# Kernel tuning notes

Measured on AMD Instinct MI355X. Metric: run time of the kernel, lower is better.

## Reference

```python
import jax, jax.numpy as jnp
import numpy as np

D_MODEL = 1024
K = 256
AMPLITUDE_MAX = 3.0
GATE_BIAS_INIT = 0.65  # alpha-gate bias initialized at logit(0.65)


def setup_inputs() -> dict:
    key = jax.random.key(0)
    k0, k1, k2, k3 = jax.random.split(key, 4)
    B, n = 4, 4096
    x = jax.random.normal(k0, (B, n, D_MODEL), dtype=jnp.float32)
    # OscillatorProjection: Linear(d_model -> 6K), chunks [A, omega, phi, alpha, g, beta]
    W_proj = jax.random.normal(k1, (6 * K, D_MODEL), dtype=jnp.float32) * 0.02
    b_proj = jnp.zeros((6 * K,), dtype=jnp.float32)
    alpha_bias = float(np.log(GATE_BIAS_INIT / (1.0 - GATE_BIAS_INIT)))
    b_proj = b_proj.at[3 * K:4 * K].set(alpha_bias)
    W_res = jax.random.normal(k2, (D_MODEL, 4 * K - 2), dtype=jnp.float32) * 0.002
    W_phase = jax.random.normal(k3, (K, D_MODEL), dtype=jnp.float32) * 0.001
    b_phase = jnp.zeros((K,), dtype=jnp.float32)
    return {
        "x": x, "W_proj": W_proj, "b_proj": b_proj, "W_res": W_res,
        "W_phase": W_phase, "b_phase": b_phase,
        "lambda_pcg": jnp.float32(0.1), "res_scale": jnp.float32(0.05),
    }


def _scan_combine(c1, c2):
    # first-order linear recurrence r_t = a_t * r_{t-1} + b_t (complex, split re/im)
    a1, br1, bi1 = c1
    a2, br2, bi2 = c2
    return (a1 * a2, a2 * br1 + br2, a2 * bi1 + bi2)


def _forward(x, W_proj, b_proj, W_res, W_phase, b_phase, lambda_pcg, res_scale):
    B, n, _ = x.shape
    # OscillatorProjection
    proj = jnp.einsum('bnd,kd->bnk', x, W_proj) + b_proj  # (B, n, 6K)
    a_raw, w_raw, p_raw, al_raw, g_raw, be_raw = jnp.split(proj, 6, axis=-1)
    A = AMPLITUDE_MAX * jax.nn.sigmoid(a_raw)
    omega = jax.nn.softplus(w_raw)
    phi = p_raw
    alpha = jax.nn.sigmoid(al_raw)
    g_out = jax.nn.sigmoid(g_raw)
    beta = jax.nn.sigmoid(be_raw)

    # phase_mode == 'log'
    positions = jnp.log1p(jnp.arange(n, dtype=jnp.float32)).reshape(1, n, 1)
    angle = omega * positions + phi
    cos_a = jnp.cos(angle)
    sin_a = jnp.sin(angle)
    one_m_a = 1.0 - alpha
    drive_r = one_m_a * A * cos_a
    drive_i = one_m_a * A * sin_a

    # parallel associative prefix scan over sequence axis
    _, r_r, r_i = jax.lax.associative_scan(_scan_combine, (alpha, drive_r, drive_i), axis=1)

    # erase (read-and-subtract)
    readout = r_r * cos_a + r_i * sin_a
    r_r = r_r - beta * readout * cos_a
    r_i = r_i - beta * readout * sin_a

    # state norm: r /= max(|r|, 1)
    modulus = jnp.sqrt(r_r * r_r + r_i * r_i + 1e-8)
    scale = jnp.maximum(modulus, 1.0)
    r_r = r_r / scale
    r_i = r_i / scale

    # demodulate: rho = r * exp(-j * angle)
    rho_re = r_r * cos_a + r_i * sin_a
    rho_im = -r_r * sin_a + r_i * cos_a

    # phase-coherence gate
    rho_norm = jnp.sqrt(rho_re * rho_re + rho_im * rho_im + 1e-8)
    phase_query = jnp.einsum('bnd,kd->bnk', x, W_phase) + b_phase
    phase_alignment = (rho_re / rho_norm) * jnp.cos(phase_query) + (rho_im / rho_norm) * jnp.sin(phase_query)
    phase_gate = jax.nn.sigmoid(lambda_pcg * phase_alignment)
    rho_re = phase_gate * rho_re
    rho_im = phase_gate * rho_im

    # SCPM: neighbor complex cross-products
    xcross_re = rho_re[:, :, :-1] * rho_re[:, :, 1:] - rho_im[:, :, :-1] * rho_im[:, :, 1:]
    xcross_im = rho_re[:, :, :-1] * rho_im[:, :, 1:] + rho_im[:, :, :-1] * rho_re[:, :, 1:]
    rho_base = jnp.concatenate([rho_re, rho_im], axis=-1)              # (B, n, 2K)
    g_base = jnp.concatenate([g_out, g_out], axis=-1)
    g_cross = 0.5 * (g_out[:, :, :-1] + g_out[:, :, 1:])
    xcross = jnp.concatenate([xcross_re, xcross_im], axis=-1)          # (B, n, 2K-2)
    g_cross_full = jnp.concatenate([g_cross, g_cross], axis=-1)
    rho = jnp.concatenate([g_base * rho_base, g_cross_full * xcross], axis=-1)  # (B, n, 4K-2)

    # eval mode: warmup_factor == 1.0
    return res_scale * jnp.einsum('bnk,dk->bnd', rho, W_res)


def reference(x, W_proj, b_proj, W_res, W_phase, b_phase, lambda_pcg, res_scale):
    return _forward(x, W_proj, b_proj, W_res, W_phase, b_phase, lambda_pcg, res_scale)
```

## Files before the change

kernel.cpp:

```cpp
#include <hip/hip_runtime.h>
#include <cmath>

#define D_MODEL 1024
#define KOSC    256
#define NSEQ    4096
#define BATCH   4
#define NROW    (BATCH * NSEQ)
#define JTOT    1792

typedef short      s16x8 __attribute__((ext_vector_type(8)));
typedef float      f32x4 __attribute__((ext_vector_type(4)));

#define GL2LDS(gsrc, ldst)                                                      \
  __builtin_amdgcn_global_load_lds(                                             \
      (const __attribute__((address_space(1))) unsigned int*)(gsrc),            \
      (__attribute__((address_space(3))) unsigned int*)(ldst), 16, 0, 0)

__device__ __forceinline__ float sigm(float x) {
    return 1.0f / (1.0f + expf(-x));
}
__device__ __forceinline__ float softplusf_(float x) {
    return fmaxf(x, 0.0f) + log1pf(expf(-fabsf(x)));
}

__device__ __forceinline__ void bf16_split(float f, unsigned short& hi,
                                           unsigned short& lo) {
    unsigned u = __float_as_uint(f);
    unsigned r = u + 0x7FFFu + ((u >> 16) & 1u);
    hi = (unsigned short)(r >> 16);
    float fh = __uint_as_float((unsigned)hi << 16);
    float fl = f - fh;
    unsigned ul = __float_as_uint(fl);
    unsigned rl = ul + 0x7FFFu + ((ul >> 16) & 1u);
    lo = (unsigned short)(rl >> 16);
}

__global__ __launch_bounds__(256) void split_x_kernel(
    const float* __restrict__ x, unsigned short* __restrict__ XH,
    unsigned short* __restrict__ XL)
{
    int i = blockIdx.x * 256 + threadIdx.x;
    float4 v = ((const float4*)x)[i];
    ushort4 h, l;
    bf16_split(v.x, h.x, l.x);
    bf16_split(v.y, h.y, l.y);
    bf16_split(v.z, h.z, l.z);
    bf16_split(v.w, h.w, l.w);
    ((ushort4*)XH)[i] = h;
    ((ushort4*)XL)[i] = l;
}

__global__ __launch_bounds__(256) void split_w_kernel(
    const float* __restrict__ Wproj, const float* __restrict__ Wphase,
    unsigned short* __restrict__ WH, unsigned short* __restrict__ WL)
{
    int i = blockIdx.x * 256 + threadIdx.x;
    int elem = i << 2;
    int row = elem >> 10;
    int col = elem & 1023;
    const float* src = (row < 1536) ? (Wproj + (size_t)row * 1024 + col)
                                    : (Wphase + (size_t)(row - 1536) * 1024 + col);
    float4 v = *(const float4*)src;
    ushort4 h, l;
    bf16_split(v.x, h.x, l.x);
    bf16_split(v.y, h.y, l.y);
    bf16_split(v.z, h.z, l.z);
    bf16_split(v.w, h.w, l.w);
    ((ushort4*)WH)[i] = h;
    ((ushort4*)WL)[i] = l;
}

__global__ __launch_bounds__(256) void pack_wres_kernel(
    const float* __restrict__ Wres, unsigned short* __restrict__ WPH)
{
    int idx = blockIdx.x * 256 + threadIdx.x;
    int d = idx >> 10;
    int j = idx & 1023;
    float v = (j < 1022) ? Wres[(size_t)d * 1022 + j] : 0.0f;
    unsigned u = __float_as_uint(v);
    unsigned r = u + 0x7FFFu + ((u >> 16) & 1u);
    WPH[idx] = (unsigned short)(r >> 16);
}

__global__ __launch_bounds__(256, 2) void gemm1_full_kernel(
    const unsigned short* __restrict__ WH, const unsigned short* __restrict__ WL,
    const unsigned short* __restrict__ XH, const unsigned short* __restrict__ XL,
    const float* __restrict__ bproj, float* __restrict__ PT)
{
    __shared__ __attribute__((aligned(16))) unsigned short AH[8192];
    __shared__ __attribute__((aligned(16))) unsigned short AL[8192];
    __shared__ __attribute__((aligned(16))) unsigned short BH[8192];
    __shared__ __attribute__((aligned(16))) unsigned short BL[8192];

    const int tid  = threadIdx.x;
    const int lane = tid & 63;
    const int w    = tid >> 6;
    const int wm   = w >> 1, wn = w & 1;
    const int m0   = (blockIdx.y + 2) * 128;
    const int n0   = blockIdx.x * 128;
    const int fr   = lane & 15;
    const int fq   = lane >> 4;

    f32x4 acc[4][4];
    #pragma unroll
    for (int i = 0; i < 4; i++)
        #pragma unroll
        for (int j = 0; j < 4; j++) acc[i][j] = (f32x4){0.f, 0.f, 0.f, 0.f};

    auto STAGE = [&](int buf, int kc) {
        const int kbase = kc * 32;
        #pragma unroll
        for (int t = 0; t < 2; t++) {
            int G  = w * 128 + t * 64 + lane;
            int gm = G & 127;
            int gq = G >> 7;
            size_t offA = (size_t)(m0 + gm) * 1024 + kbase + gq * 8;
            size_t offB = (size_t)(n0 + gm) * 1024 + kbase + gq * 8;
            int ldsg = buf * 4096 + (w * 128 + t * 64) * 8;
            GL2LDS(WH + offA, &AH[ldsg]);
            GL2LDS(WL + offA, &AL[ldsg]);
            GL2LDS(XH + offB, &BH[ldsg]);
            GL2LDS(XL + offB, &BL[ldsg]);
        }
    };

    STAGE(0, 0);
    __syncthreads();

    for (int kc = 0; kc < 32; kc++) {
        const int cur = kc & 1;
        if (kc + 1 < 32) STAGE(cur ^ 1, kc + 1);

        s16x8 ah[4], al[4], bh[4], bl[4];
        #pragma unroll
        for (int f = 0; f < 4; f++) {
            int aoff = cur * 4096 + (fq * 128 + wm * 64 + f * 16 + fr) * 8;
            int boff = cur * 4096 + (fq * 128 + wn * 64 + f * 16 + fr) * 8;
            ah[f] = *(const s16x8*)&AH[aoff];
            al[f] = *(const s16x8*)&AL[aoff];
            bh[f] = *(const s16x8*)&BH[boff];
            bl[f] = *(const s16x8*)&BL[boff];
        }
        __builtin_amdgcn_s_setprio(1);
        #pragma unroll
        for (int i = 0; i < 4; i++)
            #pragma unroll
            for (int j = 0; j < 4; j++) {
                acc[i][j] = __builtin_amdgcn_mfma_f32_16x16x32_bf16(ah[i], bh[j], acc[i][j], 0, 0, 0);
                acc[i][j] = __builtin_amdgcn_mfma_f32_16x16x32_bf16(ah[i], bl[j], acc[i][j], 0, 0, 0);
                acc[i][j] = __builtin_amdgcn_mfma_f32_16x16x32_bf16(al[i], bh[j], acc[i][j], 0, 0, 0);
            }
        __builtin_amdgcn_s_setprio(0);
        __syncthreads();
    }

    #pragma unroll
    for (int i = 0; i < 4; i++) {
        int mbase = m0 + wm * 64 + i * 16 + fq * 4;
        #pragma unroll
        for (int j = 0; j < 4; j++) {
            int n = n0 + wn * 64 + j * 16 + fr;
            #pragma unroll
            for (int rg = 0; rg < 4; rg++) {
                int m = mbase + rg;
                PT[(size_t)m * NROW + n] = acc[i][j][rg] + bproj[m];
            }
        }
    }
}

__global__ __launch_bounds__(256, 2) void gemm1_lite_kernel(
    const unsigned short* __restrict__ WH, const unsigned short* __restrict__ XH,
    const float* __restrict__ bproj, const float* __restrict__ bphase,
    float* __restrict__ PT)
{
    __shared__ __attribute__((aligned(16))) unsigned short AH[16384];
    __shared__ __attribute__((aligned(16))) unsigned short BH[16384];

    const int tid  = threadIdx.x;
    const int lane = tid & 63;
    const int w    = tid >> 6;
    const int wm   = w >> 1, wn = w & 1;
    const int yt   = blockIdx.y;
    const int jt   = (yt < 2) ? yt : yt + 4;
    const int m0   = jt * 128;
    const int n0   = blockIdx.x * 128;
    const int fr   = lane & 15;
    const int fq   = lane >> 4;

    f32x4 acc[4][4];
    #pragma unroll
    for (int i = 0; i < 4; i++)
        #pragma unroll
        for (int j = 0; j < 4; j++) acc[i][j] = (f32x4){0.f, 0.f, 0.f, 0.f};

    auto STAGE = [&](int buf, int kc) {
        const int kbase = kc * 64;
        #pragma unroll
        for (int t = 0; t < 4; t++) {
            int G  = t * 256 + tid;
            int gm = G & 127;
            int gq = G >> 7;
            size_t offA = (size_t)(m0 + gm) * 1024 + kbase + gq * 8;
            size_t offB = (size_t)(n0 + gm) * 1024 + kbase + gq * 8;
            int ldsg = buf * 8192 + (t * 256 + w * 64) * 8;
            GL2LDS(WH + offA, &AH[ldsg]);
            GL2LDS(XH + offB, &BH[ldsg]);
        }
    };

    STAGE(0, 0);
    __syncthreads();

    for (int kc = 0; kc < 16; kc++) {
        const int cur = kc & 1;
        if (kc + 1 < 16) STAGE(cur ^ 1, kc + 1);

        #pragma unroll
        for (int s = 0; s < 2; s++) {
            s16x8 ah[4], bh[4];
            #pragma unroll
            for (int f = 0; f < 4; f++) {
                int aoff = cur * 8192 + (((s * 4 + fq) * 128) + wm * 64 + f * 16 + fr) * 8;
                int boff = cur * 8192 + (((s * 4 + fq) * 128) + wn * 64 + f * 16 + fr) * 8;
                ah[f] = *(const s16x8*)&AH[aoff];
                bh[f] = *(const s16x8*)&BH[boff];
            }
            __builtin_amdgcn_s_setprio(1);
            #pragma unroll
            for (int i = 0; i < 4; i++)
                #pragma unroll
                for (int j = 0; j < 4; j++)
                    acc[i][j] = __builtin_amdgcn_mfma_f32_16x16x32_bf16(ah[i], bh[j], acc[i][j], 0, 0, 0);
            __builtin_amdgcn_s_setprio(0);
        }
        __syncthreads();
    }

    #pragma unroll
    for (int i = 0; i < 4; i++) {
        int mbase = m0 + wm * 64 + i * 16 + fq * 4;
        #pragma unroll
        for (int j = 0; j < 4; j++) {
            int n = n0 + wn * 64 + j * 16 + fr;
            #pragma unroll
            for (int rg = 0; rg < 4; rg++) {
                int m = mbase + rg;
                float bias = (m < 1536) ? bproj[m] : bphase[m - 1536];
                PT[(size_t)m * NROW + n] = acc[i][j][rg] + bias;
            }
        }
    }
}

__global__ __launch_bounds__(256) void scan_kernel(float* PT,
                                                   const float* lambda_ptr)
{
    const int bx = blockIdx.x;
    const int k = bx & 255;
    const int b = bx >> 8;
    const int t = threadIdx.x;
    const size_t colb = (size_t)b * NSEQ;
    const size_t R = NROW;

    float* rowA  = PT + (size_t)(k)        * R + colb;
    float* rowW  = PT + (size_t)(256 + k)  * R + colb;
    float* rowP  = PT + (size_t)(512 + k)  * R + colb;
    float* rowAl = PT + (size_t)(768 + k)  * R + colb;
    float* rowG  = PT + (size_t)(1024 + k) * R + colb;
    float* rowBe = PT + (size_t)(1280 + k) * R + colb;
    float* rowPq = PT + (size_t)(1536 + k) * R + colb;

    __shared__ float s_al[NSEQ + 256];
    __shared__ float s_rr[NSEQ + 256];
    __shared__ float s_ri[NSEQ + 256];
    __shared__ float s_sa[256], s_sbr[256], s_sbi[256];

    const float lam = *lambda_ptr;

    float cs_r[16], sn_r[16];

    #pragma unroll
    for (int i = 0; i < 16; i++) {
        int n = i * 256 + t;
        float araw = rowA[n];
        float wraw = rowW[n];
        float praw = rowP[n];
        float alraw = rowAl[n];
        float A     = 3.0f * sigm(araw);
        float alpha = sigm(alraw);
        float omega = softplusf_(wraw);
        float ang   = fmaf(omega, log1pf((float)n), praw);
        float sn, cs;
        sincosf(ang, &sn, &cs);
        cs_r[i] = cs;
        sn_r[i] = sn;
        float amp = (1.0f - alpha) * A;
        int pidx = n + (n >> 4);
        s_al[pidx] = alpha;
        s_rr[pidx] = amp * cs;
        s_ri[pidx] = amp * sn;
    }
    __syncthreads();

    {
        float ap = 1.0f, br = 0.0f, bi = 0.0f;
        int base = t * 17;
        #pragma unroll
        for (int i = 0; i < 16; i++) {
            float a = s_al[base + i];
            br = fmaf(a, br, s_rr[base + i]);
            bi = fmaf(a, bi, s_ri[base + i]);
            ap *= a;
        }
        s_sa[t] = ap; s_sbr[t] = br; s_sbi[t] = bi;
    }
    __syncthreads();

    for (int off = 1; off < 256; off <<= 1) {
        float a2 = s_sa[t], b2r = s_sbr[t], b2i = s_sbi[t];
        float a1 = 1.0f, b1r = 0.0f, b1i = 0.0f;
        if (t >= off) { a1 = s_sa[t - off]; b1r = s_sbr[t - off]; b1i = s_sbi[t - off]; }
        __syncthreads();
        s_sa[t]  = a1 * a2;
        s_sbr[t] = fmaf(a2, b1r, b2r);
        s_sbi[t] = fmaf(a2, b1i, b2i);
        __syncthreads();
    }

    {
        float cr = 0.0f, ci = 0.0f;
        if (t > 0) { cr = s_sbr[t - 1]; ci = s_sbi[t - 1]; }
        int base = t * 17;
        #pragma unroll
        for (int i = 0; i < 16; i++) {
            float a = s_al[base + i];
            cr = fmaf(a, cr, s_rr[base + i]);
            ci = fmaf(a, ci, s_ri[base + i]);
            s_rr[base + i] = cr;
            s_ri[base + i] = ci;
        }
    }
    __syncthreads();

    #pragma unroll
    for (int i = 0; i < 16; i++) {
        int n = i * 256 + t;
        float beraw = rowBe[n];
        float graw = rowG[n];
        float pq = rowPq[n];

        float cs = cs_r[i];
        float sn = sn_r[i];

        int pidx = n + (n >> 4);
        float rr = s_rr[pidx], ri = s_ri[pidx];
        float beta = sigm(beraw);
        float g = sigm(graw);

        float readout = rr * cs + ri * sn;
        rr -= beta * readout * cs;
        ri -= beta * readout * sn;

        float modulus = sqrtf(rr * rr + ri * ri + 1e-8f);
        float scale = fmaxf(modulus, 1.0f);
        rr /= scale; ri /= scale;

        float rho_re = rr * cs + ri * sn;
        float rho_im = -rr * sn + ri * cs;

        float rho_norm = sqrtf(rho_re * rho_re + rho_im * rho_im + 1e-8f);
        float sq, cq;
        sincosf(pq, &sq, &cq);
        float pa = (rho_re * cq + rho_im * sq) / rho_norm;
        float gate = sigm(lam * pa);
        rho_re *= gate;
        rho_im *= gate;

        rowA[n] = rho_re;
        rowW[n] = rho_im;
        rowP[n] = g;
    }
}

__global__ __launch_bounds__(256) void pack_rho_kernel(
    const float* __restrict__ PT, unsigned short* __restrict__ RTH,
    unsigned short* __restrict__ RTL)
{
    __shared__ float s_re[256 * 33];
    __shared__ float s_im[256 * 33];
    __shared__ float s_g [256 * 33];

    const int tid = threadIdx.x;
    const int r0 = blockIdx.x * 32;

    {
        int lr = tid & 31;
        int k0 = tid >> 5;
        for (int it = 0; it < 32; it++) {
            int k = it * 8 + k0;
            size_t go = (size_t)k * NROW + r0 + lr;
            s_re[k * 33 + lr] = PT[go];
            s_im[k * 33 + lr] = PT[(size_t)256 * NROW + go];
            s_g [k * 33 + lr] = PT[(size_t)512 * NROW + go];
        }
    }
    __syncthreads();

    const int r = tid >> 3;
    const int c = tid & 7;
    for (int i = 0; i < 16; i++) {
        int jb = (c + 8 * i) * 8;
        unsigned short h[8], l[8];
        #pragma unroll
        for (int e = 0; e < 8; e++) {
            int j = jb + e;
            float v;
            if (j < 256) {
                v = s_g[j * 33 + r] * s_re[j * 33 + r];
            } else if (j < 512) {
                int k = j - 256;
                v = s_g[k * 33 + r] * s_im[k * 33 + r];
            } else if (j < 767) {
                int k = j - 512;
                float gc = 0.5f * (s_g[k * 33 + r] + s_g[(k + 1) * 33 + r]);
                v = gc * (s_re[k * 33 + r] * s_re[(k + 1) * 33 + r]
                        - s_im[k * 33 + r] * s_im[(k + 1) * 33 + r]);
            } else if (j < 1022) {
                int k = j - 767;
                float gc = 0.5f * (s_g[k * 33 + r] + s_g[(k + 1) * 33 + r]);
                v = gc * (s_re[k * 33 + r] * s_im[(k + 1) * 33 + r]
                        + s_im[k * 33 + r] * s_re[(k + 1) * 33 + r]);
            } else {
                v = 0.0f;
            }
            bf16_split(v, h[e], l[e]);
        }
        size_t off = (size_t)(r0 + r) * 1024 + jb;
        s16x8 hv, lv;
        #pragma unroll
        for (int e = 0; e < 8; e++) { hv[e] = (short)h[e]; lv[e] = (short)l[e]; }
        *(s16x8*)&RTH[off] = hv;
        *(s16x8*)&RTL[off] = lv;
    }
}

__global__ __launch_bounds__(256, 3) void gemm2_kernel(
    const unsigned short* __restrict__ WPH,
    const unsigned short* __restrict__ RTH, const unsigned short* __restrict__ RTL,
    const float* __restrict__ rs_ptr, float* __restrict__ out)
{
    __shared__ __attribute__((aligned(16))) unsigned short AH[8192];
    __shared__ __attribute__((aligned(16))) unsigned short BH[8192];
    __shared__ __attribute__((aligned(16))) unsigned short BL[8192];

    const int tid  = threadIdx.x;
    const int lane = tid & 63;
    const int w    = tid >> 6;
    const int wm   = w >> 1, wn = w & 1;
    const int m0   = blockIdx.y * 128;
    const int n0   = blockIdx.x * 128;
    const int fr   = lane & 15;
    const int fq   = lane >> 4;
    const float rs = *rs_ptr;

    f32x4 acc[4][4];
    #pragma unroll
    for (int i = 0; i < 4; i++)
        #pragma unroll
        for (int j = 0; j < 4; j++) acc[i][j] = (f32x4){0.f, 0.f, 0.f, 0.f};

    auto STAGE = [&](int buf, int kc) {
        const int kbase = kc * 32;
        #pragma unroll
        for (int t = 0; t < 2; t++) {
            int G  = w * 128 + t * 64 + lane;
            int gm = G & 127;
            int gq = G >> 7;
            size_t offA = (size_t)(m0 + gm) * 1024 + kbase + gq * 8;
            size_t offB = (size_t)(n0 + gm) * 1024 + kbase + gq * 8;
            int ldsg = buf * 4096 + (w * 128 + t * 64) * 8;
            GL2LDS(WPH + offA, &AH[ldsg]);
            GL2LDS(RTH + offB, &BH[ldsg]);
            GL2LDS(RTL + offB, &BL[ldsg]);
        }
    };

    STAGE(0, 0);
    __syncthreads();

    for (int kc = 0; kc < 32; kc++) {
        const int cur = kc & 1;
        if (kc + 1 < 32) STAGE(cur ^ 1, kc + 1);

        s16x8 ah[4], bh[4], bl[4];
        #pragma unroll
        for (int f = 0; f < 4; f++) {
            int aoff = cur * 4096 + (fq * 128 + wm * 64 + f * 16 + fr) * 8;
            int boff = cur * 4096 + (fq * 128 + wn * 64 + f * 16 + fr) * 8;
            ah[f] = *(const s16x8*)&AH[aoff];
            bh[f] = *(const s16x8*)&BH[boff];
            bl[f] = *(const s16x8*)&BL[boff];
        }
        __builtin_amdgcn_s_setprio(1);
        #pragma unroll
        for (int i = 0; i < 4; i++)
            #pragma unroll
            for (int j = 0; j < 4; j++) {
                acc[i][j] = __builtin_amdgcn_mfma_f32_16x16x32_bf16(ah[i], bh[j], acc[i][j], 0, 0, 0);
                acc[i][j] = __builtin_amdgcn_mfma_f32_16x16x32_bf16(ah[i], bl[j], acc[i][j], 0, 0, 0);
            }
        __builtin_amdgcn_s_setprio(0);
        __syncthreads();
    }

    #pragma unroll
    for (int i = 0; i < 4; i++) {
        int d = m0 + wm * 64 + i * 16 + fq * 4;
        #pragma unroll
        for (int j = 0; j < 4; j++) {
            int n = n0 + wn * 64 + j * 16 + fr;
            float4 v = { rs * acc[i][j][0], rs * acc[i][j][1],
                         rs * acc[i][j][2], rs * acc[i][j][3] };
            *(float4*)&out[(size_t)n * 1024 + d] = v;
        }
    }
}

extern "C" void kernel_launch(void* const* d_in, const int* in_sizes, int n_in,
                              void* d_out, int out_size, void* d_ws, size_t ws_size,
                              hipStream_t stream)
{
    const float* x      = (const float*)d_in[0];
    const float* Wproj  = (const float*)d_in[1];
    const float* bproj  = (const float*)d_in[2];
    const float* Wres   = (const float*)d_in[3];
    const float* Wphase = (const float*)d_in[4];
    const float* bphase = (const float*)d_in[5];
    const float* lam    = (const float*)d_in[6];
    const float* rs     = (const float*)d_in[7];
    float* out = (float*)d_out;

    float* PT = (float*)d_ws;
    unsigned short* WH  = (unsigned short*)((char*)d_ws + (size_t)JTOT * NROW * 4);
    unsigned short* WL  = WH + (size_t)JTOT * 1024;
    unsigned short* RTH = (unsigned short*)(PT + (size_t)768 * NROW);
    unsigned short* RTL = RTH + (size_t)NROW * 1024;
    unsigned short* WPH = (unsigned short*)PT;
    unsigned short* XH  = (unsigned short*)d_out;
    unsigned short* XL  = XH + (size_t)NROW * 1024;

    hipLaunchKernelGGL(split_x_kernel, dim3(NROW * D_MODEL / 1024), dim3(256), 0, stream,
                       x, XH, XL);
    hipLaunchKernelGGL(split_w_kernel, dim3(JTOT * D_MODEL / 1024), dim3(256), 0, stream,
                       Wproj, Wphase, WH, WL);
    hipLaunchKernelGGL(gemm1_full_kernel, dim3(NROW / 128, 4), dim3(256), 0, stream,
                       WH, WL, XH, XL, bproj, PT);
    hipLaunchKernelGGL(gemm1_lite_kernel, dim3(NROW / 128, 10), dim3(256), 0, stream,
                       WH, XH, bproj, bphase, PT);
    hipLaunchKernelGGL(scan_kernel, dim3(BATCH * KOSC), dim3(256), 0, stream,
                       PT, lam);
    hipLaunchKernelGGL(pack_rho_kernel, dim3(NROW / 32), dim3(256), 0, stream,
                       PT, RTH, RTL);
    hipLaunchKernelGGL(pack_wres_kernel, dim3(1024 * 1024 / 256), dim3(256), 0, stream,
                       Wres, WPH);
    hipLaunchKernelGGL(gemm2_kernel, dim3(NROW / 128, 1024 / 128), dim3(256), 0, stream,
                       WPH, RTH, RTL, rs, out);
}
```

Measured before the change: 534.2 us.

## Enlarge GEMM tiles to 512 threads with triple-buffered LDS pipelining

All three GEMM kernels now run 512-thread blocks. Tiles grow to 256x128 for the full-precision GEMM and to 256x256 for the lite GEMM and the output GEMM. The two-buffer loop with a sync every step is replaced by a three-stage LDS ring, synchronised with explicit vmcnt waits and bare barriers, so global-to-LDS loads run two steps ahead of the MFMA work. Larger tiles cut global traffic per FLOP and the deeper pipeline hides load latency. The cost is much more LDS per block (up to 144KB), larger accumulator register use, and fewer blocks in the grid.

Result: slower. 706.5 us (+32.3%).

```diff
diff --git a/kernel.cpp b/kernel.cpp
--- a/kernel.cpp
+++ b/kernel.cpp
@@ -15,6 +15,8 @@
   __builtin_amdgcn_global_load_lds(                                             \
       (const __attribute__((address_space(1))) unsigned int*)(gsrc),            \
       (__attribute__((address_space(3))) unsigned int*)(ldst), 16, 0, 0)
+
+#define MFMA16(a, b, c) __builtin_amdgcn_mfma_f32_16x16x32_bf16((a), (b), (c), 0, 0, 0)
 
 __device__ __forceinline__ float sigm(float x) {
     return 1.0f / (1.0f + expf(-x));
@@ -82,21 +84,20 @@
     WPH[idx] = (unsigned short)(r >> 16);
 }
 
-__global__ __launch_bounds__(256, 2) void gemm1_full_kernel(
+
+__global__ __launch_bounds__(512, 2) void gemm1_full_kernel(
     const unsigned short* __restrict__ WH, const unsigned short* __restrict__ WL,
     const unsigned short* __restrict__ XH, const unsigned short* __restrict__ XL,
     const float* __restrict__ bproj, float* __restrict__ PT)
 {
-    __shared__ __attribute__((aligned(16))) unsigned short AH[8192];
-    __shared__ __attribute__((aligned(16))) unsigned short AL[8192];
-    __shared__ __attribute__((aligned(16))) unsigned short BH[8192];
-    __shared__ __attribute__((aligned(16))) unsigned short BL[8192];
+    __shared__ __attribute__((aligned(16))) unsigned short smem[3 * 24576];
 
     const int tid  = threadIdx.x;
     const int lane = tid & 63;
     const int w    = tid >> 6;
-    const int wm   = w >> 1, wn = w & 1;
-    const int m0   = (blockIdx.y + 2) * 128;
+    const int wm   = w >> 1;
+    const int wn   = w & 1;
+    const int m0   = (blockIdx.y + 1) * 256;
     const int n0   = blockIdx.x * 128;
     const int fr   = lane & 15;
     const int fq   = lane >> 4;
@@ -107,52 +108,71 @@
         #pragma unroll
         for (int j = 0; j < 4; j++) acc[i][j] = (f32x4){0.f, 0.f, 0.f, 0.f};
 
-    auto STAGE = [&](int buf, int kc) {
-        const int kbase = kc * 32;
-        #pragma unroll
-        for (int t = 0; t < 2; t++) {
-            int G  = w * 128 + t * 64 + lane;
-            int gm = G & 127;
-            int gq = G >> 7;
-            size_t offA = (size_t)(m0 + gm) * 1024 + kbase + gq * 8;
-            size_t offB = (size_t)(n0 + gm) * 1024 + kbase + gq * 8;
-            int ldsg = buf * 4096 + (w * 128 + t * 64) * 8;
-            GL2LDS(WH + offA, &AH[ldsg]);
-            GL2LDS(WL + offA, &AL[ldsg]);
-            GL2LDS(XH + offB, &BH[ldsg]);
-            GL2LDS(XL + offB, &BL[ldsg]);
+    auto STAGE = [&](int b, int t) {
+        const int kb = t * 32;
+        const int base = b * 24576;
+        #pragma unroll
+        for (int it = 0; it < 2; it++) {
+            int G   = it * 512 + tid;
+            int row = G & 255;
+            int gq  = G >> 8;
+            size_t offA = (size_t)(m0 + row) * 1024 + kb + gq * 8;
+            int gb = (it * 512 + w * 64) * 8;
+            GL2LDS(WH + offA, &smem[base + gb]);
+            GL2LDS(WL + offA, &smem[base + 8192 + gb]);
+        }
+        {
+            int G   = tid;
+            int row = G & 127;
+            int gq  = G >> 7;
+            size_t offB = (size_t)(n0 + row) * 1024 + kb + gq * 8;
+            int gb = (w * 64) * 8;
+            GL2LDS(XH + offB, &smem[base + 16384 + gb]);
+            GL2LDS(XL + offB, &smem[base + 20480 + gb]);
         }
     };
 
-    STAGE(0, 0);
-    __syncthreads();
-
-    for (int kc = 0; kc < 32; kc++) {
-        const int cur = kc & 1;
-        if (kc + 1 < 32) STAGE(cur ^ 1, kc + 1);
-
+    auto TILE = [&](int b) {
+        const int base = b * 24576;
         s16x8 ah[4], al[4], bh[4], bl[4];
         #pragma unroll
-        for (int f = 0; f < 4; f++) {
-            int aoff = cur * 4096 + (fq * 128 + wm * 64 + f * 16 + fr) * 8;
-            int boff = cur * 4096 + (fq * 128 + wn * 64 + f * 16 + fr) * 8;
-            ah[f] = *(const s16x8*)&AH[aoff];
-            al[f] = *(const s16x8*)&AL[aoff];
-            bh[f] = *(const s16x8*)&BH[boff];
-            bl[f] = *(const s16x8*)&BL[boff];
+        for (int i = 0; i < 4; i++) {
+            int g = (fq * 256 + wm * 64 + i * 16 + fr) * 8;
+            ah[i] = *(const s16x8*)&smem[base + g];
+            al[i] = *(const s16x8*)&smem[base + 8192 + g];
+        }
+        #pragma unroll
+        for (int j = 0; j < 4; j++) {
+            int g = (fq * 128 + wn * 64 + j * 16 + fr) * 8;
+            bh[j] = *(const s16x8*)&smem[base + 16384 + g];
+            bl[j] = *(const s16x8*)&smem[base + 20480 + g];
         }
         __builtin_amdgcn_s_setprio(1);
         #pragma unroll
         for (int i = 0; i < 4; i++)
             #pragma unroll
             for (int j = 0; j < 4; j++) {
-                acc[i][j] = __builtin_amdgcn_mfma_f32_16x16x32_bf16(ah[i], bh[j], acc[i][j], 0, 0, 0);
-                acc[i][j] = __builtin_amdgcn_mfma_f32_16x16x32_bf16(ah[i], bl[j], acc[i][j], 0, 0, 0);
-                acc[i][j] = __builtin_amdgcn_mfma_f32_16x16x32_bf16(al[i], bh[j], acc[i][j], 0, 0, 0);
+                acc[i][j] = MFMA16(ah[i], bh[j], acc[i][j]);
+                acc[i][j] = MFMA16(ah[i], bl[j], acc[i][j]);
+                acc[i][j] = MFMA16(al[i], bh[j], acc[i][j]);
             }
         __builtin_amdgcn_s_setprio(0);
-        __syncthreads();
-    }
+    };
+
+    STAGE(0, 0);
+    STAGE(1, 1);
+    int bc = 0, bs = 2;
+    for (int t = 0; t < 31; t++) {
+        asm volatile("s_waitcnt vmcnt(6)" ::: "memory");
+        __builtin_amdgcn_s_barrier();
+        if (t < 30) STAGE(bs, t + 2);
+        TILE(bc);
+        bc = (bc == 2) ? 0 : bc + 1;
+        bs = (bs == 2) ? 0 : bs + 1;
+    }
+    asm volatile("s_waitcnt vmcnt(0)" ::: "memory");
+    __builtin_amdgcn_s_barrier();
+    TILE(bc);
 
     #pragma unroll
     for (int i = 0; i < 4; i++) {
@@ -169,77 +189,82 @@
     }
 }
 
-__global__ __launch_bounds__(256, 2) void gemm1_lite_kernel(
+__global__ __launch_bounds__(512, 2) void gemm1_lite_kernel(
     const unsigned short* __restrict__ WH, const unsigned short* __restrict__ XH,
     const float* __restrict__ bproj, const float* __restrict__ bphase,
     float* __restrict__ PT)
 {
-    __shared__ __attribute__((aligned(16))) unsigned short AH[16384];
-    __shared__ __attribute__((aligned(16))) unsigned short BH[16384];
+    __shared__ __attribute__((aligned(16))) unsigned short smem[3 * 16384];
 
     const int tid  = threadIdx.x;
     const int lane = tid & 63;
     const int w    = tid >> 6;
-    const int wm   = w >> 1, wn = w & 1;
+    const int wm   = w >> 2;
+    const int wn   = w & 3;
     const int yt   = blockIdx.y;
-    const int jt   = (yt < 2) ? yt : yt + 4;
-    const int m0   = jt * 128;
-    const int n0   = blockIdx.x * 128;
+    const int m0   = (yt == 0) ? 0 : (512 + yt * 256);
+    const int n0   = blockIdx.x * 256;
     const int fr   = lane & 15;
     const int fq   = lane >> 4;
 
-    f32x4 acc[4][4];
-    #pragma unroll
-    for (int i = 0; i < 4; i++)
+    f32x4 acc[8][4];
+    #pragma unroll
+    for (int i = 0; i < 8; i++)
         #pragma unroll
         for (int j = 0; j < 4; j++) acc[i][j] = (f32x4){0.f, 0.f, 0.f, 0.f};
 
-    auto STAGE = [&](int buf, int kc) {
-        const int kbase = kc * 64;
-        #pragma unroll
-        for (int t = 0; t < 4; t++) {
-            int G  = t * 256 + tid;
-            int gm = G & 127;
-            int gq = G >> 7;
-            size_t offA = (size_t)(m0 + gm) * 1024 + kbase + gq * 8;
-            size_t offB = (size_t)(n0 + gm) * 1024 + kbase + gq * 8;
-            int ldsg = buf * 8192 + (t * 256 + w * 64) * 8;
-            GL2LDS(WH + offA, &AH[ldsg]);
-            GL2LDS(XH + offB, &BH[ldsg]);
+    auto STAGE = [&](int b, int t) {
+        const int kb = t * 32;
+        const int base = b * 16384;
+        #pragma unroll
+        for (int it = 0; it < 2; it++) {
+            int G   = it * 512 + tid;
+            int row = G & 255;
+            int gq  = G >> 8;
+            size_t offA = (size_t)(m0 + row) * 1024 + kb + gq * 8;
+            size_t offB = (size_t)(n0 + row) * 1024 + kb + gq * 8;
+            int gb = (it * 512 + w * 64) * 8;
+            GL2LDS(WH + offA, &smem[base + gb]);
+            GL2LDS(XH + offB, &smem[base + 8192 + gb]);
         }
     };
 
+    auto TILE = [&](int b) {
+        const int base = b * 16384;
+        s16x8 ah[8], bh[4];
+        #pragma unroll
+        for (int i = 0; i < 8; i++)
+            ah[i] = *(const s16x8*)&smem[base + (fq * 256 + wm * 128 + i * 16 + fr) * 8];
+        #pragma unroll
+        for (int j = 0; j < 4; j++)
+            bh[j] = *(const s16x8*)&smem[base + 8192 + (fq * 256 + wn * 64 + j * 16 + fr) * 8];
+        __builtin_amdgcn_s_setprio(1);
+        #pragma unroll
+        for (int i = 0; i < 8; i++)
+            #pragma unroll
+            for (int j = 0; j < 4; j++)
+                acc[i][j] = MFMA16(ah[i], bh[j], acc[i][j]);
+        __builtin_amdgcn_s_setprio(0);
+    };
+
     STAGE(0, 0);
-    __syncthreads();
-
-    for (int kc = 0; kc < 16; kc++) {
-        const int cur = kc & 1;
-        if (kc + 1 < 16) STAGE(cur ^ 1, kc + 1);
-
-        #pragma unroll
-        for (int s = 0; s < 2; s++) {
-            s16x8 ah[4], bh[4];
-            #pragma unroll
-            for (int f = 0; f < 4; f++) {
-                int aoff = cur * 8192 + (((s * 4 + fq) * 128) + wm * 64 + f * 16 + fr) * 8;
-                int boff = cur * 8192 + (((s * 4 + fq) * 128) + wn * 64 + f * 16 + fr) * 8;
-                ah[f] = *(const s16x8*)&AH[aoff];
-                bh[f] = *(const s16x8*)&BH[boff];
-            }
-            __builtin_amdgcn_s_setprio(1);
-            #pragma unroll
-            for (int i = 0; i < 4; i++)
-                #pragma unroll
-                for (int j = 0; j < 4; j++)
-                    acc[i][j] = __builtin_amdgcn_mfma_f32_16x16x32_bf16(ah[i], bh[j], acc[i][j], 0, 0, 0);
-            __builtin_amdgcn_s_setprio(0);
-        }
-        __syncthreads();
-    }
-
-    #pragma unroll
-    for (int i = 0; i < 4; i++) {
-        int mbase = m0 + wm * 64 + i * 16 + fq * 4;
+    STAGE(1, 1);
+    int bc = 0, bs = 2;
+    for (int t = 0; t < 31; t++) {
+        asm volatile("s_waitcnt vmcnt(4)" ::: "memory");
+        __builtin_amdgcn_s_barrier();
+        if (t < 30) STAGE(bs, t + 2);
+        TILE(bc);
+        bc = (bc == 2) ? 0 : bc + 1;
+        bs = (bs == 2) ? 0 : bs + 1;
+    }
+    asm volatile("s_waitcnt vmcnt(0)" ::: "memory");
+    __builtin_amdgcn_s_barrier();
+    TILE(bc);
+
+    #pragma unroll
+    for (int i = 0; i < 8; i++) {
+        int mbase = m0 + wm * 128 + i * 16 + fq * 4;
         #pragma unroll
         for (int j = 0; j < 4; j++) {
             int n = n0 + wn * 64 + j * 16 + fr;
@@ -445,78 +470,88 @@
     }
 }
 
-__global__ __launch_bounds__(256, 3) void gemm2_kernel(
+__global__ __launch_bounds__(512, 2) void gemm2_kernel(
     const unsigned short* __restrict__ WPH,
     const unsigned short* __restrict__ RTH, const unsigned short* __restrict__ RTL,
     const float* __restrict__ rs_ptr, float* __restrict__ out)
 {
-    __shared__ __attribute__((aligned(16))) unsigned short AH[8192];
-    __shared__ __attribute__((aligned(16))) unsigned short BH[8192];
-    __shared__ __attribute__((aligned(16))) unsigned short BL[8192];
+    __shared__ __attribute__((aligned(16))) unsigned short smem[3 * 24576];
 
     const int tid  = threadIdx.x;
     const int lane = tid & 63;
     const int w    = tid >> 6;
-    const int wm   = w >> 1, wn = w & 1;
-    const int m0   = blockIdx.y * 128;
-    const int n0   = blockIdx.x * 128;
+    const int wm   = w >> 2;
+    const int wn   = w & 3;
+    const int m0   = blockIdx.y * 256;
+    const int n0   = blockIdx.x * 256;
     const int fr   = lane & 15;
     const int fq   = lane >> 4;
     const float rs = *rs_ptr;
 
-    f32x4 acc[4][4];
-    #pragma unroll
-    for (int i = 0; i < 4; i++)
+    f32x4 acc[8][4];
+    #pragma unroll
+    for (int i = 0; i < 8; i++)
         #pragma unroll
         for (int j = 0; j < 4; j++) acc[i][j] = (f32x4){0.f, 0.f, 0.f, 0.f};
 
-    auto STAGE = [&](int buf, int kc) {
-        const int kbase = kc * 32;
-        #pragma unroll
-        for (int t = 0; t < 2; t++) {
-            int G  = w * 128 + t * 64 + lane;
-            int gm = G & 127;
-            int gq = G >> 7;
-            size_t offA = (size_t)(m0 + gm) * 1024 + kbase + gq * 8;
-            size_t offB = (size_t)(n0 + gm) * 1024 + kbase + gq * 8;
-            int ldsg = buf * 4096 + (w * 128 + t * 64) * 8;
-            GL2LDS(WPH + offA, &AH[ldsg]);
-            GL2LDS(RTH + offB, &BH[ldsg]);
-            GL2LDS(RTL + offB, &BL[ldsg]);
+    auto STAGE = [&](int b, int t) {
+        const int kb = t * 32;
+        const int base = b * 24576;
+        #pragma unroll
+        for (int it = 0; it < 2; it++) {
+            int G   = it * 512 + tid;
+            int row = G & 255;
+            int gq  = G >> 8;
+            size_t offA = (size_t)(m0 + row) * 1024 + kb + gq * 8;
+            size_t offB = (size_t)(n0 + row) * 1024 + kb + gq * 8;
+            int gb = (it * 512 + w * 64) * 8;
+            GL2LDS(WPH + offA, &smem[base + gb]);
+            GL2LDS(RTH + offB, &smem[base + 8192 + gb]);
+            GL2LDS(RTL + offB, &smem[base + 16384 + gb]);
         }
     };
 
-    STAGE(0, 0);
-    __syncthreads();
-
-    for (int kc = 0; kc < 32; kc++) {
-        const int cur = kc & 1;
-        if (kc + 1 < 32) STAGE(cur ^ 1, kc + 1);
-
-        s16x8 ah[4], bh[4], bl[4];
-        #pragma unroll
-        for (int f = 0; f < 4; f++) {
-            int aoff = cur * 4096 + (fq * 128 + wm * 64 + f * 16 + fr) * 8;
-            int boff = cur * 4096 + (fq * 128 + wn * 64 + f * 16 + fr) * 8;
-            ah[f] = *(const s16x8*)&AH[aoff];
-            bh[f] = *(const s16x8*)&BH[boff];
-            bl[f] = *(const s16x8*)&BL[boff];
+    auto TILE = [&](int b) {
+        const int base = b * 24576;
+        s16x8 ah[8], bh[4], bl[4];
+        #pragma unroll
+        for (int i = 0; i < 8; i++)
+            ah[i] = *(const s16x8*)&smem[base + (fq * 256 + wm * 128 + i * 16 + fr) * 8];
+        #pragma unroll
+        for (int j = 0; j < 4; j++) {
+            int g = (fq * 256 + wn * 64 + j * 16 + fr) * 8;
+            bh[j] = *(const s16x8*)&smem[base + 8192 + g];
+            bl[j] = *(const s16x8*)&smem[base + 16384 + g];
         }
         __builtin_amdgcn_s_setprio(1);
         #pragma unroll
-        for (int i = 0; i < 4; i++)
+        for (int i = 0; i < 8; i++)
             #pragma unroll
             for (int j = 0; j < 4; j++) {
-                acc[i][j] = __builtin_amdgcn_mfma_f32_16x16x32_bf16(ah[i], bh[j], acc[i][j], 0, 0, 0);
-                acc[i][j] = __builtin_amdgcn_mfma_f32_16x16x32_bf16(ah[i], bl[j], acc[i][j], 0, 0, 0);
+                acc[i][j] = MFMA16(ah[i], bh[j], acc[i][j]);
+                acc[i][j] = MFMA16(ah[i], bl[j], acc[i][j]);
             }
         __builtin_amdgcn_s_setprio(0);
-        __syncthreads();
-    }
-
-    #pragma unroll
-    for (int i = 0; i < 4; i++) {
-        int d = m0 + wm * 64 + i * 16 + fq * 4;
+    };
+
+    STAGE(0, 0);
+    STAGE(1, 1);
+    int bc = 0, bs = 2;
+    for (int t = 0; t < 31; t++) {
+        asm volatile("s_waitcnt vmcnt(6)" ::: "memory");
+        __builtin_amdgcn_s_barrier();
+        if (t < 30) STAGE(bs, t + 2);
+        TILE(bc);
+        bc = (bc == 2) ? 0 : bc + 1;
+        bs = (bs == 2) ? 0 : bs + 1;
+    }
+    asm volatile("s_waitcnt vmcnt(0)" ::: "memory");
+    __builtin_amdgcn_s_barrier();
+    TILE(bc);
+
+    #pragma unroll
+    for (int i = 0; i < 8; i++) {
+        int d = m0 + wm * 128 + i * 16 + fq * 4;
         #pragma unroll
         for (int j = 0; j < 4; j++) {
             int n = n0 + wn * 64 + j * 16 + fr;
@@ -554,9 +589,9 @@
                        x, XH, XL);
     hipLaunchKernelGGL(split_w_kernel, dim3(JTOT * D_MODEL / 1024), dim3(256), 0, stream,
                        Wproj, Wphase, WH, WL);
-    hipLaunchKernelGGL(gemm1_full_kernel, dim3(NROW / 128, 4), dim3(256), 0, stream,
+    hipLaunchKernelGGL(gemm1_full_kernel, dim3(NROW / 128, 2), dim3(512), 0, stream,
                        WH, WL, XH, XL, bproj, PT);
-    hipLaunchKernelGGL(gemm1_lite_kernel, dim3(NROW / 128, 10), dim3(256), 0, stream,
+    hipLaunchKernelGGL(gemm1_lite_kernel, dim3(NROW / 256, 5), dim3(512), 0, stream,
                        WH, XH, bproj, bphase, PT);
     hipLaunchKernelGGL(scan_kernel, dim3(BATCH * KOSC), dim3(256), 0, stream,
                        PT, lam);
@@ -564,6 +599,6 @@
                        PT, RTH, RTL);
     hipLaunchKernelGGL(pack_wres_kernel, dim3(1024 * 1024 / 256), dim3(256), 0, stream,
                        Wres, WPH);
-    hipLaunchKernelGGL(gemm2_kernel, dim3(NROW / 128, 1024 / 128), dim3(256), 0, stream,
+    hipLaunchKernelGGL(gemm2_kernel, dim3(NROW / 256, 1024 / 256), dim3(512), 0, stream,
                        WPH, RTH, RTL, rs, out);
 }
```
